# Optimization experiments

Measured on AMD Instinct MI355X. Metric: run time of the kernel, lower is better.

Reference implementation:

```python
import jax, jax.numpy as jnp
import numpy as np

D = 8192          # Hadamard dimension (power of 2)
K = 1024          # number of selected columns = len(idx)
NORMALIZED = True
SCALE = np.float32(1.0 / np.sqrt(D))


def setup_inputs() -> dict:
    key = jax.random.key(0)
    k1, k2 = jax.random.split(key)
    u = jax.random.normal(k1, (4, 2048, K), dtype=jnp.float32)
    idx = jnp.sort(jax.random.randint(k2, (K,), 0, D, dtype=jnp.int32))
    return {"u": u, "idx": idx}


def _fwht(x):
    """Unnormalized fast Walsh-Hadamard transform over last dim. x: (B, D)."""
    B, d = x.shape
    h = 1
    while h < d:  # log2(D) static iterations -> jit-friendly
        y = x.reshape(B, d // (2 * h), 2, h)
        a, b = y[:, :, 0, :], y[:, :, 1, :]
        x = jnp.stack([a + b, a - b], axis=2).reshape(B, d)
        h *= 2
    return x


def reference(u, idx):
    # x = H_D[:, idx] @ u  (optionally / sqrt(D))
    # = FWHT(scatter(u at idx into zeros(D))) since H @ e_j = H[:, j]
    orig = u.shape[:-1]
    u2 = u.reshape(-1, u.shape[-1])                      # (B, K)
    z = jnp.zeros((u2.shape[0], D), u.dtype).at[:, idx].add(u2)  # (B, D)
    out = _fwht(z)
    if NORMALIZED:
        out = out * SCALE
    return out.reshape(*orig, D)
```

## Files before the change

### kernel.cpp

```cpp
#include <hip/hip_runtime.h>

#define D      8192
#define K      1024
#define BLOCK  256
#define SCALE  0.011048543456039806f

__device__ __forceinline__ int swz(int i) {
    return i ^ (((i >> 8) & 31) << 3);
}

__device__ __forceinline__ void fwht32(float* x) {
#pragma unroll
    for (int s = 0; s < 5; ++s) {
        const int h = 1 << s;
#pragma unroll
        for (int g = 0; g < 32; g += 2 * h)
#pragma unroll
            for (int e = 0; e < h; ++e) {
                float a = x[g + e], b = x[g + e + h];
                x[g + e]     = a + b;
                x[g + e + h] = a - b;
            }
    }
}

__device__ __forceinline__ void fwht8(float* x) {
#pragma unroll
    for (int s = 0; s < 3; ++s) {
        const int h = 1 << s;
#pragma unroll
        for (int g = 0; g < 8; g += 2 * h)
#pragma unroll
            for (int e = 0; e < h; ++e) {
                float a = x[g + e], b = x[g + e + h];
                x[g + e]     = a + b;
                x[g + e + h] = a - b;
            }
    }
}

__global__ __launch_bounds__(BLOCK, 4)
void UpProjectFastHadamardTransform_80101140070867_kernel(
    const float* __restrict__ u, const int* __restrict__ idx,
    float* __restrict__ out)
{
    __shared__ float lds[D];
    const int row = blockIdx.x;
    const int t   = threadIdx.x;

    float4* lds4 = (float4*)lds;
#pragma unroll
    for (int j = 0; j < D / 4 / BLOCK; ++j)
        lds4[t + j * BLOCK] = make_float4(0.f, 0.f, 0.f, 0.f);
    __syncthreads();

    {
        const float4* urow4 = (const float4*)(u + (size_t)row * K);
        const int4*   idx4  = (const int4*)idx;
        float4 v  = urow4[t];
        int4   id = idx4[t];
        atomicAdd(&lds[swz(id.x)], v.x);
        atomicAdd(&lds[swz(id.y)], v.y);
        atomicAdd(&lds[swz(id.z)], v.z);
        atomicAdd(&lds[swz(id.w)], v.w);
    }
    __syncthreads();

    float x[32];

#pragma unroll
    for (int g = 0; g < 4; ++g) {
        const int p = swz(t * 32 + g * 8);
        float4 a = *(const float4*)&lds[p];
        float4 b = *(const float4*)&lds[p + 4];
        x[g * 8 + 0] = a.x; x[g * 8 + 1] = a.y; x[g * 8 + 2] = a.z; x[g * 8 + 3] = a.w;
        x[g * 8 + 4] = b.x; x[g * 8 + 5] = b.y; x[g * 8 + 6] = b.z; x[g * 8 + 7] = b.w;
    }
    fwht32(x);
#pragma unroll
    for (int g = 0; g < 4; ++g) {
        const int p = swz(t * 32 + g * 8);
        *(float4*)&lds[p]     = make_float4(x[g*8+0], x[g*8+1], x[g*8+2], x[g*8+3]);
        *(float4*)&lds[p + 4] = make_float4(x[g*8+4], x[g*8+5], x[g*8+6], x[g*8+7]);
    }
    __syncthreads();

    {
        const int hi3 = t >> 5, lo5 = t & 31;
        const int base = hi3 * 1024 + lo5;
#pragma unroll
        for (int r = 0; r < 32; ++r) x[r] = lds[swz(base + r * 32)];
        fwht32(x);
#pragma unroll
        for (int r = 0; r < 32; ++r) lds[swz(base + r * 32)] = x[r];
    }
    __syncthreads();

#pragma unroll
    for (int g = 0; g < 4; ++g)
#pragma unroll
        for (int r = 0; r < 8; ++r)
            x[g * 8 + r] = lds[swz(r * 1024 + g * 256 + t)];
#pragma unroll
    for (int g = 0; g < 4; ++g) fwht8(&x[g * 8]);

    float* orow = out + (size_t)row * D;
#pragma unroll
    for (int g = 0; g < 4; ++g)
#pragma unroll
        for (int r = 0; r < 8; ++r)
            orow[r * 1024 + g * 256 + t] = x[g * 8 + r] * SCALE;
}

extern "C" void kernel_launch(void* const* d_in, const int* in_sizes, int n_in,
                              void* d_out, int out_size, void* d_ws, size_t ws_size,
                              hipStream_t stream) {
    const float* u   = (const float*)d_in[0];
    const int*   idx = (const int*)d_in[1];
    float*       out = (float*)d_out;
    const int rows = in_sizes[0] / K;
    hipLaunchKernelGGL(UpProjectFastHadamardTransform_80101140070867_kernel,
                       dim3(rows), dim3(BLOCK), 0, stream, u, idx, out);
}
```

Before: 334.5 us.

## Restructure FWHT stages as transpose passes with float4 LDS reads and vector stores

Reorganizes the in-LDS Hadamard transform so every stage reads contiguous float4 chunks with an XOR swizzle, then writes back transposed scalars. This replaces the strided scalar column pass and the per-element swizzle. The final output is written as float4 stores instead of scalar stores. The global loads of u and idx are hoisted before the LDS zeroing, and occupancy is raised to 5 blocks per SIMD. In exchange it adds extra barriers and a third LDS round trip.

New measurement: 302.2 us. 9.7% less time.

```diff
diff --git a/kernel.cpp b/kernel.cpp
--- a/kernel.cpp
+++ b/kernel.cpp
@@ -5,9 +5,7 @@
 #define BLOCK  256
 #define SCALE  0.011048543456039806f
 
-__device__ __forceinline__ int swz(int i) {
-    return i ^ (((i >> 8) & 31) << 3);
-}
+__device__ __forceinline__ int swz4(int f) { return f ^ ((f >> 3) & 7); }
 
 __device__ __forceinline__ void fwht32(float* x) {
 #pragma unroll
@@ -39,77 +37,74 @@
     }
 }
 
-__global__ __launch_bounds__(BLOCK, 4)
+__global__ __launch_bounds__(BLOCK, 5)
 void UpProjectFastHadamardTransform_80101140070867_kernel(
     const float* __restrict__ u, const int* __restrict__ idx,
     float* __restrict__ out)
 {
-    __shared__ float lds[D];
+    __shared__ float4 lds4[D / 4];
+    float* lds = (float*)lds4;
     const int row = blockIdx.x;
     const int t   = threadIdx.x;
 
-    float4* lds4 = (float4*)lds;
+    const float4 v  = ((const float4*)(u + (size_t)row * K))[t];
+    const int4   id = ((const int4*)idx)[t];
+
 #pragma unroll
     for (int j = 0; j < D / 4 / BLOCK; ++j)
         lds4[t + j * BLOCK] = make_float4(0.f, 0.f, 0.f, 0.f);
     __syncthreads();
 
     {
-        const float4* urow4 = (const float4*)(u + (size_t)row * K);
-        const int4*   idx4  = (const int4*)idx;
-        float4 v  = urow4[t];
-        int4   id = idx4[t];
-        atomicAdd(&lds[swz(id.x)], v.x);
-        atomicAdd(&lds[swz(id.y)], v.y);
-        atomicAdd(&lds[swz(id.z)], v.z);
-        atomicAdd(&lds[swz(id.w)], v.w);
+        int f, a;
+        f = id.x >> 2; a = 4 * swz4(f) + (id.x & 3); atomicAdd(&lds[a], v.x);
+        f = id.y >> 2; a = 4 * swz4(f) + (id.y & 3); atomicAdd(&lds[a], v.y);
+        f = id.z >> 2; a = 4 * swz4(f) + (id.z & 3); atomicAdd(&lds[a], v.z);
+        f = id.w >> 2; a = 4 * swz4(f) + (id.w & 3); atomicAdd(&lds[a], v.w);
     }
     __syncthreads();
 
     float x[32];
+    const int c  = t & 7;
+    const int wb = 4 * ((t >> 2) ^ ((t >> 5) & 7)) + (t & 3);
 
 #pragma unroll
-    for (int g = 0; g < 4; ++g) {
-        const int p = swz(t * 32 + g * 8);
-        float4 a = *(const float4*)&lds[p];
-        float4 b = *(const float4*)&lds[p + 4];
-        x[g * 8 + 0] = a.x; x[g * 8 + 1] = a.y; x[g * 8 + 2] = a.z; x[g * 8 + 3] = a.w;
-        x[g * 8 + 4] = b.x; x[g * 8 + 5] = b.y; x[g * 8 + 6] = b.z; x[g * 8 + 7] = b.w;
+    for (int g = 0; g < 8; ++g) {
+        float4 a = lds4[t * 8 + (g ^ c)];
+        x[4*g+0] = a.x; x[4*g+1] = a.y; x[4*g+2] = a.z; x[4*g+3] = a.w;
     }
     fwht32(x);
+    __syncthreads();
 #pragma unroll
-    for (int g = 0; g < 4; ++g) {
-        const int p = swz(t * 32 + g * 8);
-        *(float4*)&lds[p]     = make_float4(x[g*8+0], x[g*8+1], x[g*8+2], x[g*8+3]);
-        *(float4*)&lds[p + 4] = make_float4(x[g*8+4], x[g*8+5], x[g*8+6], x[g*8+7]);
-    }
-    __syncthreads();
-
-    {
-        const int hi3 = t >> 5, lo5 = t & 31;
-        const int base = hi3 * 1024 + lo5;
-#pragma unroll
-        for (int r = 0; r < 32; ++r) x[r] = lds[swz(base + r * 32)];
-        fwht32(x);
-#pragma unroll
-        for (int r = 0; r < 32; ++r) lds[swz(base + r * 32)] = x[r];
-    }
+    for (int j = 0; j < 32; ++j) lds[j * 256 + wb] = x[j];
     __syncthreads();
 
 #pragma unroll
-    for (int g = 0; g < 4; ++g)
+    for (int g = 0; g < 8; ++g) {
+        float4 a = lds4[t * 8 + (g ^ c)];
+        x[4*g+0] = a.x; x[4*g+1] = a.y; x[4*g+2] = a.z; x[4*g+3] = a.w;
+    }
+    fwht32(x);
+    __syncthreads();
 #pragma unroll
-        for (int r = 0; r < 8; ++r)
-            x[g * 8 + r] = lds[swz(r * 1024 + g * 256 + t)];
+    for (int j = 0; j < 32; ++j) lds[j * 256 + wb] = x[j];
+    __syncthreads();
+
 #pragma unroll
-    for (int g = 0; g < 4; ++g) fwht8(&x[g * 8]);
+    for (int g = 0; g < 8; ++g) {
+        float4 a = lds4[t * 8 + (g ^ c)];
+        x[4*g+0] = a.x; x[4*g+1] = a.y; x[4*g+2] = a.z; x[4*g+3] = a.w;
+    }
+#pragma unroll
+    for (int g2 = 0; g2 < 4; ++g2) fwht8(&x[g2 * 8]);
 
-    float* orow = out + (size_t)row * D;
+    float* orow = out + (size_t)row * D + ((t >> 3) * 32 + (t & 7) * 4);
 #pragma unroll
-    for (int g = 0; g < 4; ++g)
-#pragma unroll
-        for (int r = 0; r < 8; ++r)
-            orow[r * 1024 + g * 256 + t] = x[g * 8 + r] * SCALE;
+    for (int e = 0; e < 8; ++e) {
+        float4 o = make_float4(x[e] * SCALE, x[8 + e] * SCALE,
+                               x[16 + e] * SCALE, x[24 + e] * SCALE);
+        *(float4*)(orow + e * 1024) = o;
+    }
 }
 
 extern "C" void kernel_launch(void* const* d_in, const int* in_sizes, int n_in,
```
